# Optimization experiments

Hardware: AMD Instinct MI355X
Metric: run time of the kernel (lower is better)

The kernel has to match this reference:

```python
import jax, jax.numpy as jnp
import numpy as np
from jax import lax


def setup_inputs() -> dict:
    key = jax.random.key(0)
    ks = jax.random.split(key, 8)
    B, S, H, L = 64, 512, 768, 9
    hidden = jax.random.normal(ks[0], (B, S, H), jnp.float32)
    label = jax.random.randint(ks[1], (B, S), 0, L, dtype=jnp.int32)
    mask = jnp.ones((B, S), jnp.int32)
    W = jax.random.normal(ks[2], (H, L), jnp.float32) * 0.02
    b = jnp.zeros((L,), jnp.float32)
    start_transitions = jax.random.normal(ks[3], (L,), jnp.float32) * 0.1
    end_transitions = jax.random.normal(ks[4], (L,), jnp.float32) * 0.1
    transitions = jax.random.normal(ks[5], (L, L), jnp.float32) * 0.1
    return dict(hidden=hidden, label=label, mask=mask, W=W, b=b,
                start_transitions=start_transitions,
                end_transitions=end_transitions,
                transitions=transitions)


def reference(hidden, label, mask, W, b, start_transitions, end_transitions, transitions):
    B, S, H = hidden.shape
    L = b.shape[0]
    # output_layer: [B,S,H] @ [H,L] -> emissions, then transpose to time-major [S,B,L]
    emissions = jnp.einsum('bsh,hl->bsl', hidden, W) + b
    em = jnp.transpose(emissions, (1, 0, 2))        # [S, B, L]
    tags = label.T                                   # [S, B]
    m = mask.T.astype(jnp.float32)                   # [S, B]

    def gather_tag(em_t, tag_t):
        # em_t [B,L], tag_t [B] -> [B]
        return jnp.take_along_axis(em_t, tag_t[:, None], axis=1)[:, 0]

    # ---- numerator: score of the gold path ----
    score0 = start_transitions[tags[0]] + gather_tag(em[0], tags[0])
    def num_step(carry, x):
        score, prev = carry
        em_t, tag_t, m_t = x
        s = transitions[prev, tag_t] + gather_tag(em_t, tag_t)
        score = score + s * m_t
        prev = jnp.where(m_t > 0, tag_t, prev)
        return (score, prev), None
    (score, last_gold), _ = lax.scan(num_step, (score0, tags[0]), (em[1:], tags[1:], m[1:]))
    score = score + end_transitions[last_gold]

    # ---- denominator: forward algorithm (logsumexp DP) ----
    alpha0 = start_transitions[None, :] + em[0]      # [B, L]
    def fwd_step(alpha, x):
        em_t, m_t = x
        nxt = jax.nn.logsumexp(alpha[:, :, None] + transitions[None, :, :] + em_t[:, None, :], axis=1)
        alpha = jnp.where(m_t[:, None] > 0, nxt, alpha)
        return alpha, None
    alphaT, _ = lax.scan(fwd_step, alpha0, (em[1:], m[1:]))
    logZ = jax.nn.logsumexp(alphaT + end_transitions[None, :], axis=1)

    llh = jnp.sum(score - logZ)                      # reduction='sum'
    loss = -llh / B

    # ---- Viterbi decode (decode() is called without mask -> full length) ----
    v0 = start_transitions[None, :] + em[0]
    def vit_step(v, em_t):
        scores = v[:, :, None] + transitions[None, :, :] + em_t[:, None, :]  # [B, L, L]
        return jnp.max(scores, axis=1), jnp.argmax(scores, axis=1)
    vT, hist = lax.scan(vit_step, v0, em[1:])        # hist [S-1, B, L]
    last_tag = jnp.argmax(vT + end_transitions[None, :], axis=1)  # [B]
    def back_step(tag, bp_t):
        prev = jnp.take_along_axis(bp_t, tag[:, None], axis=1)[:, 0]
        return prev, prev
    _, prevs = lax.scan(back_step, last_tag, hist, reverse=True)  # [S-1, B]
    path = jnp.concatenate([prevs, last_tag[None, :]], axis=0).T  # [B, S]

    # ---- accuracy bookkeeping (label > 0 mask) ----
    label_flat = label.reshape(-1)
    label_mask = (label_flat > 0).astype(jnp.int32)
    predict = path.reshape(-1).astype(jnp.int32) * label_mask
    correct = jnp.sum((predict == label_flat).astype(jnp.float32))
    return loss, correct, predict, label_flat
```

## Files before the change

### kernel.cpp

```cpp
#include <hip/hip_runtime.h>
#include <hip/hip_bf16.h>

#define NB 64
#define NS 512
#define NH 768
#define NL 9
#define NROWS (NB*NS)
#define EMN (NROWS*NL)

__device__ __forceinline__ float readlane_f(float v, int l) {
    return __int_as_float(__builtin_amdgcn_readlane(__float_as_int(v), l));
}
__device__ __forceinline__ unsigned long long readlane_u64(unsigned long long v, int l) {
    unsigned int lo = (unsigned int)__builtin_amdgcn_readlane((int)(unsigned int)(v & 0xffffffffULL), l);
    unsigned int hi = (unsigned int)__builtin_amdgcn_readlane((int)(unsigned int)(v >> 32), l);
    return ((unsigned long long)hi << 32) | (unsigned long long)lo;
}
template <int CTRL>
__device__ __forceinline__ float dpp_add(float x) {
    int t = __builtin_amdgcn_update_dpp(0, __float_as_int(x), CTRL, 0xf, 0xf, false);
    return x + __int_as_float(t);
}
__device__ __forceinline__ float wave_sum_to63(float x) {
    x = dpp_add<0x111>(x);
    x = dpp_add<0x112>(x);
    x = dpp_add<0x114>(x);
    x = dpp_add<0x118>(x);
    x = dpp_add<0x142>(x);
    x = dpp_add<0x143>(x);
    return x;
}

__global__ __launch_bounds__(256) void k_gemm(const float* __restrict__ hidden,
                                              const float* __restrict__ W,
                                              const float* __restrict__ bias,
                                              float* __restrict__ em,
                                              float* __restrict__ out) {
    __shared__ float s_part[4][4][NL];
    int tid = threadIdx.x;
    int lane = tid & 63;
    int w = tid >> 6;
    int bx = blockIdx.x;
    if (bx == 0 && tid == 0) { out[0] = 0.f; out[1] = 0.f; }

    int kbase = 192 * w + lane;
    float Wv[3][NL];
#pragma unroll
    for (int c = 0; c < 3; c++) {
        const float* wp = W + (size_t)(kbase + 64 * c) * NL;
#pragma unroll
        for (int j = 0; j < NL; j++) Wv[c][j] = wp[j];
    }

#pragma unroll
    for (int r = 0; r < 4; r++) {
        int row = 4 * bx + r;
        const float* hp = hidden + (size_t)row * NH + kbase;
        float h0 = hp[0], h1 = hp[64], h2 = hp[128];
        float acc[NL];
#pragma unroll
        for (int j = 0; j < NL; j++) {
            acc[j] = fmaf(h0, Wv[0][j], fmaf(h1, Wv[1][j], h2 * Wv[2][j]));
        }
#pragma unroll
        for (int j = 0; j < NL; j++) acc[j] = wave_sum_to63(acc[j]);
        if (lane == 63) {
#pragma unroll
            for (int j = 0; j < NL; j++) s_part[w][r][j] = acc[j];
        }
    }
    __syncthreads();
    if (tid < 36) {
        int r = tid / NL, j = tid % NL;
        float v = (s_part[0][r][j] + s_part[1][r][j]) +
                  (s_part[2][r][j] + s_part[3][r][j]) + bias[j];
        em[(size_t)(4 * bx + r) * NL + j] = v;
    }
}

__global__ __launch_bounds__(256) void k_dp(const float* __restrict__ em,
                                            const int* __restrict__ label,
                                            const int* __restrict__ mask,
                                            const float* __restrict__ startT,
                                            const float* __restrict__ endT,
                                            const float* __restrict__ trans,
                                            float* __restrict__ out) {
    __shared__ float s_em[NS * NL];
    __shared__ float s_v[NS * NL];
    __shared__ unsigned char s_bp[NS * NL];
    __shared__ unsigned char s_path[NS];
    __shared__ int s_mk[NS];
    __shared__ float s_T[NL * NL];

    int bx = blockIdx.x;
    int tid = threadIdx.x;
    int lane = tid & 63;
    int b = bx & 63;

    {
        const float4* ef = (const float4*)(em + (size_t)b * NS * NL);
        float4* sf = (float4*)s_em;
        for (int q = tid; q < NS * NL / 4; q += 256) sf[q] = ef[q];
        if (tid < NS / 4) ((int4*)s_mk)[tid] = ((const int4*)(mask + b * NS))[tid];
        if (tid < NL * NL) s_T[tid] = trans[tid];
    }
    __syncthreads();

    if (bx < NB) {
        if (tid < 64) {
            int j9 = tid < NL ? tid : NL - 1;
            float Mcol[NL];
#pragma unroll
            for (int i = 0; i < NL; i++) Mcol[i] = __expf(s_T[i * NL + j9]);
            float a = __expf(startT[j9] + s_em[j9]);
            int eacc = 0;
            float xpre[4]; int mpre[4];
#pragma unroll
            for (int p = 0; p < 4; p++) { xpre[p] = __expf(s_em[(1 + p) * NL + j9]); mpre[p] = s_mk[1 + p]; }
#pragma unroll 4
            for (int t = 1; t < NS; ++t) {
                float xev = xpre[0]; int mv = mpre[0];
                xpre[0] = xpre[1]; xpre[1] = xpre[2]; xpre[2] = xpre[3];
                mpre[0] = mpre[1]; mpre[1] = mpre[2]; mpre[2] = mpre[3];
                int tn = t + 4; tn = tn < NS ? tn : NS - 1;
                xpre[3] = __expf(s_em[tn * NL + j9]); mpre[3] = s_mk[tn];
                float p0 = readlane_f(a, 0) * Mcol[0];
                float p1 = readlane_f(a, 1) * Mcol[1];
                float p2 = readlane_f(a, 2) * Mcol[2];
                float p3 = readlane_f(a, 3) * Mcol[3];
                float p4 = readlane_f(a, 4) * Mcol[4];
                float p5 = readlane_f(a, 5) * Mcol[5];
                float p6 = readlane_f(a, 6) * Mcol[6];
                float p7 = readlane_f(a, 7) * Mcol[7];
                float p8 = readlane_f(a, 8) * Mcol[8];
                float s = (((p0 + p1) + (p2 + p3)) + ((p4 + p5) + (p6 + p7))) + p8;
                float anew = xev * s;
                a = (mv > 0) ? anew : a;
                if ((t & 7) == 0) {
                    float c0 = readlane_f(a, 0), c1 = readlane_f(a, 1), c2 = readlane_f(a, 2);
                    float c3 = readlane_f(a, 3), c4 = readlane_f(a, 4), c5 = readlane_f(a, 5);
                    float c6 = readlane_f(a, 6), c7 = readlane_f(a, 7), c8 = readlane_f(a, 8);
                    float c = (((c0 + c1) + (c2 + c3)) + ((c4 + c5) + (c6 + c7))) + c8;
                    int ex = ((__float_as_int(c) >> 23) & 255) - 127;
                    a = ldexpf(a, -ex);
                    eacc += ex;
                }
            }
            float z = a * __expf(endT[j9]);
            float c0 = readlane_f(z, 0), c1 = readlane_f(z, 1), c2 = readlane_f(z, 2);
            float c3 = readlane_f(z, 3), c4 = readlane_f(z, 4), c5 = readlane_f(z, 5);
            float c6 = readlane_f(z, 6), c7 = readlane_f(z, 7), c8 = readlane_f(z, 8);
            float c = (((c0 + c1) + (c2 + c3)) + ((c4 + c5) + (c6 + c7))) + c8;
            if (tid == 0) {
                float lz = (float)eacc * 0.6931471805599453f + __logf(c);
                atomicAdd(out, lz * (1.0f / (float)NB));
            }
        } else if (tid < 128) {
            const int* lb = label + b * NS;
            int t0 = lane * 8;
            int lab[8]; int mk[8];
#pragma unroll
            for (int r = 0; r < 8; r++) { lab[r] = lb[t0 + r]; mk[r] = s_mk[t0 + r]; }
            if (lane == 0) mk[0] = 1;
            int h = 0, sl = 0;
#pragma unroll
            for (int r = 0; r < 8; r++) { if (mk[r] > 0) { h = 1; sl = lab[r]; } }
#pragma unroll
            for (int d = 1; d < 64; d <<= 1) {
                int ho = __shfl_up(h, d);
                int so = __shfl_up(sl, d);
                if (!h) { h = ho; sl = so; }
            }
            int lg = __shfl(sl, 63);
            int incoming = __shfl_up(sl, 1);
            float sc = 0.f;
            int prevr = (lane == 0) ? lab[0] : incoming;
#pragma unroll
            for (int r = 0; r < 8; r++) {
                int t = t0 + r;
                if (t > 0) {
                    float s = s_T[prevr * NL + lab[r]] + s_em[t * NL + lab[r]];
                    sc += s * (float)mk[r];
                }
                if (mk[r] > 0) prevr = lab[r];
            }
            if (lane == 0) {
                int g0 = lab[0];
                sc += startT[g0] + s_em[g0] + endT[lg];
            }
#pragma unroll
            for (int d = 1; d < 64; d <<= 1) sc += __shfl_xor(sc, d);
            if (lane == 0) atomicAdd(out, -sc * (1.0f / (float)NB));
        }
    } else {
        if (tid < 64) {
            int j9 = tid < NL ? tid : NL - 1;
            float Tcol[NL];
#pragma unroll
            for (int i = 0; i < NL; i++) Tcol[i] = s_T[i * NL + j9];
            float v = startT[j9] + s_em[j9];
            if (tid < NL) s_v[tid] = v;
            float epre[4];
#pragma unroll
            for (int p = 0; p < 4; p++) epre[p] = s_em[(1 + p) * NL + j9];
#pragma unroll 4
            for (int t = 1; t < NS; ++t) {
                float emv = epre[0];
                epre[0] = epre[1]; epre[1] = epre[2]; epre[2] = epre[3];
                int tn = t + 4; tn = tn < NS ? tn : NS - 1;
                epre[3] = s_em[tn * NL + j9];
                float m0 = readlane_f(v, 0) + Tcol[0];
                float m1 = readlane_f(v, 1) + Tcol[1];
                float m2 = readlane_f(v, 2) + Tcol[2];
                float m3 = readlane_f(v, 3) + Tcol[3];
                float m4 = readlane_f(v, 4) + Tcol[4];
                float m5 = readlane_f(v, 5) + Tcol[5];
                float m6 = readlane_f(v, 6) + Tcol[6];
                float m7 = readlane_f(v, 7) + Tcol[7];
                float m8 = readlane_f(v, 8) + Tcol[8];
                float M = fmaxf(fmaxf(fmaxf(fmaxf(m0, m1), fmaxf(m2, m3)),
                                      fmaxf(fmaxf(m4, m5), fmaxf(m6, m7))), m8);
                v = M + emv;
                if (tid < NL) s_v[t * NL + tid] = v;
            }
        }
        __syncthreads();
#pragma unroll
        for (int rep = 0; rep < 2; rep++) {
            int t = 1 + tid + 256 * rep;
            if (t < NS) {
                float vp[NL], emt[NL];
#pragma unroll
                for (int i = 0; i < NL; i++) vp[i] = s_v[(t - 1) * NL + i];
#pragma unroll
                for (int j = 0; j < NL; j++) emt[j] = s_em[t * NL + j];
#pragma unroll
                for (int j = 0; j < NL; j++) {
                    float e = emt[j];
                    float val[NL];
#pragma unroll
                    for (int i = 0; i < NL; i++) val[i] = (vp[i] + s_T[i * NL + j]) + e;
                    bool c01 = val[0] >= val[1]; float m01 = c01 ? val[0] : val[1]; int i01 = c01 ? 0 : 1;
                    bool c23 = val[2] >= val[3]; float m23 = c23 ? val[2] : val[3]; int i23 = c23 ? 2 : 3;
                    bool c45 = val[4] >= val[5]; float m45 = c45 ? val[4] : val[5]; int i45 = c45 ? 4 : 5;
                    bool c67 = val[6] >= val[7]; float m67 = c67 ? val[6] : val[7]; int i67 = c67 ? 6 : 7;
                    bool ca = m01 >= m23; float ma = ca ? m01 : m23; int ia = ca ? i01 : i23;
                    bool cb = m45 >= m67; float mb = cb ? m45 : m67; int ib = cb ? i45 : i67;
                    bool cc = ma >= mb;  float mc = cc ? ma : mb;  int ic = cc ? ia : ib;
                    bool cd = mc >= val[8]; int bi = cd ? ic : 8;
                    s_bp[t * NL + j] = (unsigned char)bi;
                }
            } else if (t == NS) {
                s_bp[0 * NL + tid - 255] = 0;
            }
        }
        __syncthreads();
        if (tid < 64) {
            float bb = s_v[(NS - 1) * NL + 0] + endT[0]; int lt = 0;
#pragma unroll
            for (int jj = 1; jj < NL; jj++) {
                float fj = s_v[(NS - 1) * NL + jj] + endT[jj];
                if (fj > bb) { bb = fj; lt = jj; }
            }
            unsigned long long G[8];
#pragma unroll
            for (int r = 0; r < 8; r++) {
                int t0 = (lane * 8 + r) * NL;
                unsigned long long g = 0;
                if (lane == 0 && r == 0) {
                    g = 0x876543210ULL;
                } else {
#pragma unroll
                    for (int x = 0; x < NL; x++) g |= (unsigned long long)s_bp[t0 + x] << (4 * x);
                }
                G[r] = g;
            }
            unsigned long long A = 0x876543210ULL;
#pragma unroll
            for (int r = 7; r >= 0; r--) {
                unsigned long long An = 0;
#pragma unroll
                for (int x = 0; x < NL; x++) {
                    int ax = (int)((A >> (4 * x)) & 15ULL);
                    int gv = (int)((G[r] >> (4 * ax)) & 15ULL);
                    An |= (unsigned long long)gv << (4 * x);
                }
                A = An;
            }
            int e = 0; int cur = lt;
            for (int ll = 63; ll >= 0; --ll) {
                if (lane == ll) e = cur;
                unsigned long long Al = readlane_u64(A, ll);
                cur = (int)((Al >> (4 * cur)) & 15ULL);
            }
            unsigned long long pw = 0; int c2 = e;
#pragma unroll
            for (int r = 7; r >= 0; r--) {
                pw |= (unsigned long long)c2 << (8 * r);
                c2 = (int)((G[r] >> (4 * c2)) & 15ULL);
            }
            *(unsigned long long*)(s_path + lane * 8) = pw;
        }
        __syncthreads();
        const int* lb = label + b * NS;
        float cnt = 0.f;
#pragma unroll
        for (int q = 0; q < 2; q++) {
            int t = tid + q * 256;
            int idx = b * NS + t;
            int lab = lb[t];
            int p = (int)s_path[t];
            int pred = (lab > 0) ? p : 0;
            out[2 + idx] = (float)pred;
            out[2 + NROWS + idx] = (float)lab;
            cnt += (pred == lab) ? 1.f : 0.f;
        }
#pragma unroll
        for (int d = 1; d < 64; d <<= 1) cnt += __shfl_xor(cnt, d);
        if ((tid & 63) == 0) atomicAdd(out + 1, cnt);
    }
}

extern "C" void kernel_launch(void* const* d_in, const int* in_sizes, int n_in,
                              void* d_out, int out_size, void* d_ws, size_t ws_size,
                              hipStream_t stream) {
    const float* hidden = (const float*)d_in[0];
    const int*   label  = (const int*)d_in[1];
    const int*   mask   = (const int*)d_in[2];
    const float* W      = (const float*)d_in[3];
    const float* bias   = (const float*)d_in[4];
    const float* startT = (const float*)d_in[5];
    const float* endT   = (const float*)d_in[6];
    const float* trans  = (const float*)d_in[7];
    float* out = (float*)d_out;

    float* em = (float*)d_ws;

    k_gemm<<<8192, 256, 0, stream>>>(hidden, W, bias, em, out);
    k_dp<<<128, 256, 0, stream>>>(em, label, mask, startT, endT, trans, out);
}
```

Before: 214.5 us.

## Pack four sequences per wavefront in CRF DP kernel using row broadcasts

The forward and Viterbi recurrences now handle four batch sequences per wavefront, one 16-lane row each. Lane broadcasts use ds_swizzle row broadcast in place of readlane, and the DP grid shrinks from 128 to 32 blocks. Emissions are read straight from global memory with an 8-deep prefetch instead of being staged in LDS. This cuts per-step latency cost per sequence, at the price of fewer blocks, a longer tail and global-load latency on the serial chain.

```diff
diff --git a/kernel.cpp b/kernel.cpp
--- a/kernel.cpp
+++ b/kernel.cpp
@@ -7,6 +7,9 @@
 #define NL 9
 #define NROWS (NB*NS)
 #define EMN (NROWS*NL)
+
+#define VST  4617
+#define BPST 4616
 
 __device__ __forceinline__ float readlane_f(float v, int l) {
     return __int_as_float(__builtin_amdgcn_readlane(__float_as_int(v), l));
@@ -29,6 +32,10 @@
     x = dpp_add<0x142>(x);
     x = dpp_add<0x143>(x);
     return x;
+}
+template <int I>
+__device__ __forceinline__ float rowbc(float x) {
+    return __int_as_float(__builtin_amdgcn_ds_swizzle(__float_as_int(x), (I << 5) | 0x10));
 }
 
 __global__ __launch_bounds__(256) void k_gemm(const float* __restrict__ hidden,
@@ -85,155 +92,214 @@
                                             const float* __restrict__ endT,
                                             const float* __restrict__ trans,
                                             float* __restrict__ out) {
-    __shared__ float s_em[NS * NL];
-    __shared__ float s_v[NS * NL];
-    __shared__ unsigned char s_bp[NS * NL];
-    __shared__ unsigned char s_path[NS];
-    __shared__ int s_mk[NS];
     __shared__ float s_T[NL * NL];
+    __shared__ int s_mki[4][NS];
+    __shared__ float s_v[4 * VST];
+    __shared__ unsigned char s_bp[4 * BPST];
+    __shared__ unsigned char s_path[4 * NS];
 
     int bx = blockIdx.x;
     int tid = threadIdx.x;
     int lane = tid & 63;
-    int b = bx & 63;
-
-    {
-        const float4* ef = (const float4*)(em + (size_t)b * NS * NL);
-        float4* sf = (float4*)s_em;
-        for (int q = tid; q < NS * NL / 4; q += 256) sf[q] = ef[q];
-        if (tid < NS / 4) ((int4*)s_mk)[tid] = ((const int4*)(mask + b * NS))[tid];
-        if (tid < NL * NL) s_T[tid] = trans[tid];
+    bool isfwd = bx < 16;
+    int b0 = (isfwd ? bx : (bx - 16)) * 4;
+
+    if (tid < NL * NL) s_T[tid] = trans[tid];
+    if (isfwd) {
+        for (int q = tid; q < 4 * NS / 4; q += 256)
+            ((int4*)s_mki)[q] = ((const int4*)(mask + b0 * NS))[q];
     }
     __syncthreads();
 
-    if (bx < NB) {
+    if (isfwd) {
         if (tid < 64) {
-            int j9 = tid < NL ? tid : NL - 1;
-            float Mcol[NL];
-#pragma unroll
-            for (int i = 0; i < NL; i++) Mcol[i] = __expf(s_T[i * NL + j9]);
-            float a = __expf(startT[j9] + s_em[j9]);
+            int bb = lane >> 4;
+            int jcol = lane & 15;
+            int jcol9 = jcol < NL ? jcol : NL - 1;
+            const float* gp = em + (size_t)(b0 + bb) * (NS * NL) + jcol9;
+            float Mc0 = __expf(s_T[0 * NL + jcol9]);
+            float Mc1 = __expf(s_T[1 * NL + jcol9]);
+            float Mc2 = __expf(s_T[2 * NL + jcol9]);
+            float Mc3 = __expf(s_T[3 * NL + jcol9]);
+            float Mc4 = __expf(s_T[4 * NL + jcol9]);
+            float Mc5 = __expf(s_T[5 * NL + jcol9]);
+            float Mc6 = __expf(s_T[6 * NL + jcol9]);
+            float Mc7 = __expf(s_T[7 * NL + jcol9]);
+            float Mc8 = __expf(s_T[8 * NL + jcol9]);
+            float a = __expf(startT[jcol9] + gp[0]);
             int eacc = 0;
-            float xpre[4]; int mpre[4];
-#pragma unroll
-            for (int p = 0; p < 4; p++) { xpre[p] = __expf(s_em[(1 + p) * NL + j9]); mpre[p] = s_mk[1 + p]; }
-#pragma unroll 4
-            for (int t = 1; t < NS; ++t) {
-                float xev = xpre[0]; int mv = mpre[0];
-                xpre[0] = xpre[1]; xpre[1] = xpre[2]; xpre[2] = xpre[3];
-                mpre[0] = mpre[1]; mpre[1] = mpre[2]; mpre[2] = mpre[3];
-                int tn = t + 4; tn = tn < NS ? tn : NS - 1;
-                xpre[3] = __expf(s_em[tn * NL + j9]); mpre[3] = s_mk[tn];
-                float p0 = readlane_f(a, 0) * Mcol[0];
-                float p1 = readlane_f(a, 1) * Mcol[1];
-                float p2 = readlane_f(a, 2) * Mcol[2];
-                float p3 = readlane_f(a, 3) * Mcol[3];
-                float p4 = readlane_f(a, 4) * Mcol[4];
-                float p5 = readlane_f(a, 5) * Mcol[5];
-                float p6 = readlane_f(a, 6) * Mcol[6];
-                float p7 = readlane_f(a, 7) * Mcol[7];
-                float p8 = readlane_f(a, 8) * Mcol[8];
-                float s = (((p0 + p1) + (p2 + p3)) + ((p4 + p5) + (p6 + p7))) + p8;
-                float anew = xev * s;
-                a = (mv > 0) ? anew : a;
-                if ((t & 7) == 0) {
-                    float c0 = readlane_f(a, 0), c1 = readlane_f(a, 1), c2 = readlane_f(a, 2);
-                    float c3 = readlane_f(a, 3), c4 = readlane_f(a, 4), c5 = readlane_f(a, 5);
-                    float c6 = readlane_f(a, 6), c7 = readlane_f(a, 7), c8 = readlane_f(a, 8);
-                    float c = (((c0 + c1) + (c2 + c3)) + ((c4 + c5) + (c6 + c7))) + c8;
-                    int ex = ((__float_as_int(c) >> 23) & 255) - 127;
-                    a = ldexpf(a, -ex);
-                    eacc += ex;
-                }
-            }
-            float z = a * __expf(endT[j9]);
-            float c0 = readlane_f(z, 0), c1 = readlane_f(z, 1), c2 = readlane_f(z, 2);
-            float c3 = readlane_f(z, 3), c4 = readlane_f(z, 4), c5 = readlane_f(z, 5);
-            float c6 = readlane_f(z, 6), c7 = readlane_f(z, 7), c8 = readlane_f(z, 8);
+
+#define FBODY(EC_, KC_) do { \
+    float _w0=rowbc<0>(a),_w1=rowbc<1>(a),_w2=rowbc<2>(a),_w3=rowbc<3>(a),_w4=rowbc<4>(a), \
+          _w5=rowbc<5>(a),_w6=rowbc<6>(a),_w7=rowbc<7>(a),_w8=rowbc<8>(a); \
+    float _p0=_w0*Mc0,_p1=_w1*Mc1,_p2=_w2*Mc2,_p3=_w3*Mc3,_p4=_w4*Mc4, \
+          _p5=_w5*Mc5,_p6=_w6*Mc6,_p7=_w7*Mc7,_p8=_w8*Mc8; \
+    float _s=(((_p0+_p1)+(_p2+_p3))+((_p4+_p5)+(_p6+_p7)))+_p8; \
+    float _an=(EC_)*_s; \
+    a = ((KC_) > 0) ? _an : a; \
+} while (0)
+
+#define FREN() do { \
+    float _c0=rowbc<0>(a),_c1=rowbc<1>(a),_c2=rowbc<2>(a),_c3=rowbc<3>(a),_c4=rowbc<4>(a), \
+          _c5=rowbc<5>(a),_c6=rowbc<6>(a),_c7=rowbc<7>(a),_c8=rowbc<8>(a); \
+    float _cc=(((_c0+_c1)+(_c2+_c3))+((_c4+_c5)+(_c6+_c7)))+_c8; \
+    int _ex=((__float_as_int(_cc)>>23)&255)-127; \
+    a=ldexpf(a,-_ex); eacc+=_ex; \
+} while (0)
+
+            float e8[8]; int k8[8];
+#pragma unroll
+            for (int p = 0; p < 8; p++) {
+                e8[p] = __expf(gp[(1 + p) * NL]);
+                k8[p] = s_mki[bb][1 + p];
+            }
+            for (int t0 = 1; t0 <= NS - 15; t0 += 8) {
+#pragma unroll
+                for (int p = 0; p < 8; p++) {
+                    int t = t0 + p;
+                    float ec = e8[p]; int kc = k8[p];
+                    int tn = t + 8; tn = tn > NS - 1 ? NS - 1 : tn;
+                    e8[p] = __expf(gp[tn * NL]);
+                    k8[p] = s_mki[bb][tn];
+                    FBODY(ec, kc);
+                    if (p == 7) FREN();
+                }
+            }
+#pragma unroll
+            for (int p = 0; p < 7; p++) FBODY(e8[p], k8[p]);
+#undef FBODY
+#undef FREN
+            float z = a * __expf(endT[jcol9]);
+            float c0 = rowbc<0>(z), c1 = rowbc<1>(z), c2 = rowbc<2>(z);
+            float c3 = rowbc<3>(z), c4 = rowbc<4>(z), c5 = rowbc<5>(z);
+            float c6 = rowbc<6>(z), c7 = rowbc<7>(z), c8 = rowbc<8>(z);
             float c = (((c0 + c1) + (c2 + c3)) + ((c4 + c5) + (c6 + c7))) + c8;
-            if (tid == 0) {
+            if (jcol == 0) {
                 float lz = (float)eacc * 0.6931471805599453f + __logf(c);
                 atomicAdd(out, lz * (1.0f / (float)NB));
             }
         } else if (tid < 128) {
+            int g = lane >> 4;
+            int ll = lane & 15;
+            int b = b0 + g;
             const int* lb = label + b * NS;
-            int t0 = lane * 8;
-            int lab[8]; int mk[8];
-#pragma unroll
-            for (int r = 0; r < 8; r++) { lab[r] = lb[t0 + r]; mk[r] = s_mk[t0 + r]; }
-            if (lane == 0) mk[0] = 1;
+            const float* ge = em + (size_t)b * NS * NL;
             int h = 0, sl = 0;
-#pragma unroll
-            for (int r = 0; r < 8; r++) { if (mk[r] > 0) { h = 1; sl = lab[r]; } }
-#pragma unroll
-            for (int d = 1; d < 64; d <<= 1) {
-                int ho = __shfl_up(h, d);
-                int so = __shfl_up(sl, d);
+            for (int cch = 0; cch < 4; cch++) {
+                int la8[8]; int mk8[8];
+#pragma unroll
+                for (int r = 0; r < 8; r++) {
+                    int t = ll * 32 + cch * 8 + r;
+                    la8[r] = lb[t];
+                    int m = s_mki[g][t];
+                    if (t == 0) m = 1;
+                    mk8[r] = m;
+                }
+#pragma unroll
+                for (int r = 0; r < 8; r++) if (mk8[r] > 0) { h = 1; sl = la8[r]; }
+            }
+#pragma unroll
+            for (int d = 1; d < 16; d <<= 1) {
+                int ho = __shfl_up(h, d, 16);
+                int so = __shfl_up(sl, d, 16);
                 if (!h) { h = ho; sl = so; }
             }
-            int lg = __shfl(sl, 63);
-            int incoming = __shfl_up(sl, 1);
+            int lg = __shfl(sl, 15, 16);
+            int incoming = __shfl_up(sl, 1, 16);
+            int labz = lb[0];
+            int prevr = (ll == 0) ? labz : incoming;
             float sc = 0.f;
-            int prevr = (lane == 0) ? lab[0] : incoming;
-#pragma unroll
-            for (int r = 0; r < 8; r++) {
-                int t = t0 + r;
-                if (t > 0) {
-                    float s = s_T[prevr * NL + lab[r]] + s_em[t * NL + lab[r]];
-                    sc += s * (float)mk[r];
-                }
-                if (mk[r] > 0) prevr = lab[r];
-            }
-            if (lane == 0) {
-                int g0 = lab[0];
-                sc += startT[g0] + s_em[g0] + endT[lg];
-            }
-#pragma unroll
-            for (int d = 1; d < 64; d <<= 1) sc += __shfl_xor(sc, d);
-            if (lane == 0) atomicAdd(out, -sc * (1.0f / (float)NB));
+            for (int cch = 0; cch < 4; cch++) {
+                int la8[8]; int mk8[8]; float ev8[8];
+#pragma unroll
+                for (int r = 0; r < 8; r++) {
+                    int t = ll * 32 + cch * 8 + r;
+                    la8[r] = lb[t];
+                    int m = s_mki[g][t];
+                    if (t == 0) m = 1;
+                    mk8[r] = m;
+                }
+#pragma unroll
+                for (int r = 0; r < 8; r++) {
+                    int t = ll * 32 + cch * 8 + r;
+                    ev8[r] = ge[t * NL + la8[r]];
+                }
+#pragma unroll
+                for (int r = 0; r < 8; r++) {
+                    int t = ll * 32 + cch * 8 + r;
+                    if (t > 0) {
+                        float s = s_T[prevr * NL + la8[r]] + ev8[r];
+                        sc += s * (float)mk8[r];
+                    }
+                    if (mk8[r] > 0) prevr = la8[r];
+                }
+            }
+            if (ll == 0) sc += startT[labz] + ge[labz] + endT[lg];
+#pragma unroll
+            for (int d = 1; d < 16; d <<= 1) sc += __shfl_xor(sc, d, 16);
+            if (ll == 0) atomicAdd(out, -sc * (1.0f / (float)NB));
         }
     } else {
         if (tid < 64) {
-            int j9 = tid < NL ? tid : NL - 1;
-            float Tcol[NL];
-#pragma unroll
-            for (int i = 0; i < NL; i++) Tcol[i] = s_T[i * NL + j9];
-            float v = startT[j9] + s_em[j9];
-            if (tid < NL) s_v[tid] = v;
-            float epre[4];
-#pragma unroll
-            for (int p = 0; p < 4; p++) epre[p] = s_em[(1 + p) * NL + j9];
-#pragma unroll 4
-            for (int t = 1; t < NS; ++t) {
-                float emv = epre[0];
-                epre[0] = epre[1]; epre[1] = epre[2]; epre[2] = epre[3];
-                int tn = t + 4; tn = tn < NS ? tn : NS - 1;
-                epre[3] = s_em[tn * NL + j9];
-                float m0 = readlane_f(v, 0) + Tcol[0];
-                float m1 = readlane_f(v, 1) + Tcol[1];
-                float m2 = readlane_f(v, 2) + Tcol[2];
-                float m3 = readlane_f(v, 3) + Tcol[3];
-                float m4 = readlane_f(v, 4) + Tcol[4];
-                float m5 = readlane_f(v, 5) + Tcol[5];
-                float m6 = readlane_f(v, 6) + Tcol[6];
-                float m7 = readlane_f(v, 7) + Tcol[7];
-                float m8 = readlane_f(v, 8) + Tcol[8];
-                float M = fmaxf(fmaxf(fmaxf(fmaxf(m0, m1), fmaxf(m2, m3)),
-                                      fmaxf(fmaxf(m4, m5), fmaxf(m6, m7))), m8);
-                v = M + emv;
-                if (tid < NL) s_v[t * NL + tid] = v;
-            }
+            int bb = lane >> 4;
+            int jcol = lane & 15;
+            int jcol9 = jcol < NL ? jcol : NL - 1;
+            const float* gv = em + (size_t)(b0 + bb) * (NS * NL) + jcol9;
+            float Tc0 = s_T[0 * NL + jcol9];
+            float Tc1 = s_T[1 * NL + jcol9];
+            float Tc2 = s_T[2 * NL + jcol9];
+            float Tc3 = s_T[3 * NL + jcol9];
+            float Tc4 = s_T[4 * NL + jcol9];
+            float Tc5 = s_T[5 * NL + jcol9];
+            float Tc6 = s_T[6 * NL + jcol9];
+            float Tc7 = s_T[7 * NL + jcol9];
+            float Tc8 = s_T[8 * NL + jcol9];
+            float v = startT[jcol9] + gv[0];
+            int svbase = bb * VST + jcol;
+            s_v[svbase] = v;
+
+#define VBODY(EC_, T_) do { \
+    float _w0=rowbc<0>(v),_w1=rowbc<1>(v),_w2=rowbc<2>(v),_w3=rowbc<3>(v),_w4=rowbc<4>(v), \
+          _w5=rowbc<5>(v),_w6=rowbc<6>(v),_w7=rowbc<7>(v),_w8=rowbc<8>(v); \
+    float _m0=_w0+Tc0,_m1=_w1+Tc1,_m2=_w2+Tc2,_m3=_w3+Tc3,_m4=_w4+Tc4, \
+          _m5=_w5+Tc5,_m6=_w6+Tc6,_m7=_w7+Tc7,_m8=_w8+Tc8; \
+    float _Ma=fmaxf(fmaxf(_m0,_m1),_m2); \
+    float _Mb=fmaxf(fmaxf(_m3,_m4),_m5); \
+    float _Mc=fmaxf(fmaxf(_m6,_m7),_m8); \
+    v = fmaxf(fmaxf(_Ma,_Mb),_Mc) + (EC_); \
+    s_v[svbase + (T_) * NL] = v; \
+} while (0)
+
+            float e8[8];
+#pragma unroll
+            for (int p = 0; p < 8; p++) e8[p] = gv[(1 + p) * NL];
+            for (int t0 = 1; t0 <= NS - 15; t0 += 8) {
+#pragma unroll
+                for (int p = 0; p < 8; p++) {
+                    int t = t0 + p;
+                    float ec = e8[p];
+                    int tn = t + 8; tn = tn > NS - 1 ? NS - 1 : tn;
+                    e8[p] = gv[tn * NL];
+                    VBODY(ec, t);
+                }
+            }
+#pragma unroll
+            for (int p = 0; p < 7; p++) VBODY(e8[p], 505 + p);
+#undef VBODY
         }
         __syncthreads();
-#pragma unroll
-        for (int rep = 0; rep < 2; rep++) {
-            int t = 1 + tid + 256 * rep;
-            if (t < NS) {
+        for (int it = 0; it < 8; it++) {
+            int item = tid + it * 256;
+            int bb = item >> 9;
+            int t = item & (NS - 1);
+            if (t > 0) {
+                const float* vpp = s_v + bb * VST + (t - 1) * NL;
+                const float* ge = em + (size_t)(b0 + bb) * (NS * NL) + t * NL;
                 float vp[NL], emt[NL];
 #pragma unroll
-                for (int i = 0; i < NL; i++) vp[i] = s_v[(t - 1) * NL + i];
-#pragma unroll
-                for (int j = 0; j < NL; j++) emt[j] = s_em[t * NL + j];
+                for (int i = 0; i < NL; i++) vp[i] = vpp[i];
+#pragma unroll
+                for (int j = 0; j < NL; j++) emt[j] = ge[j];
 #pragma unroll
                 for (int j = 0; j < NL; j++) {
                     float e = emt[j];
@@ -248,19 +314,21 @@
                     bool cb = m45 >= m67; float mb = cb ? m45 : m67; int ib = cb ? i45 : i67;
                     bool cc = ma >= mb;  float mc = cc ? ma : mb;  int ic = cc ? ia : ib;
                     bool cd = mc >= val[8]; int bi = cd ? ic : 8;
-                    s_bp[t * NL + j] = (unsigned char)bi;
-                }
-            } else if (t == NS) {
-                s_bp[0 * NL + tid - 255] = 0;
+                    s_bp[bb * BPST + t * NL + j] = (unsigned char)bi;
+                }
             }
         }
         __syncthreads();
-        if (tid < 64) {
-            float bb = s_v[(NS - 1) * NL + 0] + endT[0]; int lt = 0;
+        {
+            int w = tid >> 6;
+            const float* sv = s_v + w * VST;
+            const unsigned char* bpp = s_bp + w * BPST;
+            unsigned char* pth = s_path + w * NS;
+            float bb2 = sv[(NS - 1) * NL + 0] + endT[0]; int lt = 0;
 #pragma unroll
             for (int jj = 1; jj < NL; jj++) {
-                float fj = s_v[(NS - 1) * NL + jj] + endT[jj];
-                if (fj > bb) { bb = fj; lt = jj; }
+                float fj = sv[(NS - 1) * NL + jj] + endT[jj];
+                if (fj > bb2) { bb2 = fj; lt = jj; }
             }
             unsigned long long G[8];
 #pragma unroll
@@ -271,7 +339,7 @@
                     g = 0x876543210ULL;
                 } else {
 #pragma unroll
-                    for (int x = 0; x < NL; x++) g |= (unsigned long long)s_bp[t0 + x] << (4 * x);
+                    for (int x = 0; x < NL; x++) g |= (unsigned long long)bpp[t0 + x] << (4 * x);
                 }
                 G[r] = g;
             }
@@ -282,15 +350,15 @@
 #pragma unroll
                 for (int x = 0; x < NL; x++) {
                     int ax = (int)((A >> (4 * x)) & 15ULL);
-                    int gv = (int)((G[r] >> (4 * ax)) & 15ULL);
-                    An |= (unsigned long long)gv << (4 * x);
+                    int gvv = (int)((G[r] >> (4 * ax)) & 15ULL);
+                    An |= (unsigned long long)gvv << (4 * x);
                 }
                 A = An;
             }
             int e = 0; int cur = lt;
-            for (int ll = 63; ll >= 0; --ll) {
-                if (lane == ll) e = cur;
-                unsigned long long Al = readlane_u64(A, ll);
+            for (int llv = 63; llv >= 0; --llv) {
+                if (lane == llv) e = cur;
+                unsigned long long Al = readlane_u64(A, llv);
                 cur = (int)((Al >> (4 * cur)) & 15ULL);
             }
             unsigned long long pw = 0; int c2 = e;
@@ -299,17 +367,19 @@
                 pw |= (unsigned long long)c2 << (8 * r);
                 c2 = (int)((G[r] >> (4 * c2)) & 15ULL);
             }
-            *(unsigned long long*)(s_path + lane * 8) = pw;
+            *(unsigned long long*)(pth + lane * 8) = pw;
         }
         __syncthreads();
-        const int* lb = label + b * NS;
         float cnt = 0.f;
 #pragma unroll
-        for (int q = 0; q < 2; q++) {
-            int t = tid + q * 256;
+        for (int q = 0; q < 8; q++) {
+            int item = tid + q * 256;
+            int bb = item >> 9;
+            int t = item & (NS - 1);
+            int b = b0 + bb;
             int idx = b * NS + t;
-            int lab = lb[t];
-            int p = (int)s_path[t];
+            int lab = label[idx];
+            int p = (int)s_path[bb * NS + t];
             int pred = (lab > 0) ? p : 0;
             out[2 + idx] = (float)pred;
             out[2 + NROWS + idx] = (float)lab;
@@ -337,5 +407,5 @@
     float* em = (float*)d_ws;
 
     k_gemm<<<8192, 256, 0, stream>>>(hidden, W, bias, em, out);
-    k_dp<<<128, 256, 0, stream>>>(em, label, mask, startT, endT, trans, out);
-}
+    k_dp<<<32, 256, 0, stream>>>(em, label, mask, startT, endT, trans, out);
+}
```

After: 210.9 us. Within noise of the previous version (-1.7%).
